# Kernel tuning notes

Measured on AMD Instinct MI355X. Metric: run time of the kernel, lower is better.

Reference implementation:

```python
import jax, jax.numpy as jnp
import numpy as np

DIM = 768
HEADS = 12
DH = DIM // HEADS  # 64


def setup_inputs() -> dict:
    key = jax.random.key(0)
    k1, k2, k3, k4, k5 = jax.random.split(key, 5)
    b, p = 16, 1024
    x = jax.random.normal(k1, (b, p, DIM), dtype=jnp.float32)
    # torch nn.Linear params: W [out, in], b [out]
    s_qkv = 1.0 / np.sqrt(DIM)
    Wqkv = jax.random.uniform(k2, (3 * DIM, DIM), jnp.float32, -s_qkv, s_qkv)
    bqkv = jax.random.uniform(k3, (3 * DIM,), jnp.float32, -s_qkv, s_qkv)
    Wo = jax.random.uniform(k4, (DIM, DIM), jnp.float32, -s_qkv, s_qkv)
    bo = jax.random.uniform(k5, (DIM,), jnp.float32, -s_qkv, s_qkv)
    return {"x": x, "Wqkv": Wqkv, "bqkv": bqkv, "Wo": Wo, "bo": bo}


def reference(x, Wqkv, bqkv, Wo, bo):
    b, p, _ = x.shape
    qkv = x @ Wqkv.T + bqkv                      # [b, p, 3*dim]
    q, k, v = jnp.split(qkv, 3, axis=-1)
    def to_heads(t):
        return t.reshape(b, p, HEADS, DH).transpose(0, 2, 1, 3)  # [b, h, p, d]
    q, k, v = to_heads(q), to_heads(k), to_heads(v)
    A = jnp.einsum('bhqd,bhkd->bhqk', q, k) / jnp.sqrt(jnp.float32(DH))
    # NOTE: softmax over the QUERY axis (dim=2), not the key axis
    P = jax.nn.softmax(A, axis=2)                # [b, h, q, k]
    MSA = jnp.einsum('bhqk,bhkd->bhqd', P, v)    # [b, h, p, d]
    MSA = MSA.transpose(0, 2, 1, 3).reshape(b, p, DIM)
    return MSA @ Wo.T + bo
```

## Files before the change

### kernel.cpp

```cpp
#include <hip/hip_runtime.h>
#include <hip/hip_bf16.h>
#include <math.h>

#define DIMC 768
#define HEADS 12
#define DHD 64
#define NB 16
#define NP 1024
#define NQKV (3*DIMC)

typedef __attribute__((ext_vector_type(8))) short bf16x8;
typedef __attribute__((ext_vector_type(4))) float f32x4;

__device__ __forceinline__ short f2bf(float f){
  unsigned u = __builtin_bit_cast(unsigned, f);
  u = (u + 0x7fffu + ((u >> 16) & 1u)) >> 16;
  return (short)u;
}
__device__ __forceinline__ float bf2f(short s){
  return __builtin_bit_cast(float, ((unsigned)(unsigned short)s) << 16);
}
__device__ __forceinline__ bf16x8 cvt8(float4 a, float4 b){
  bf16x8 v;
  v[0]=f2bf(a.x); v[1]=f2bf(a.y); v[2]=f2bf(a.z); v[3]=f2bf(a.w);
  v[4]=f2bf(b.x); v[5]=f2bf(b.y); v[6]=f2bf(b.z); v[7]=f2bf(b.w);
  return v;
}
__device__ __forceinline__ void glds16(const void* gsrc, void* ldst){
  __builtin_amdgcn_global_load_lds(
      (const __attribute__((address_space(1))) unsigned int*)gsrc,
      (__attribute__((address_space(3))) unsigned int*)ldst, 16, 0, 0);
}
__device__ __forceinline__ int xcd_swz(int p, int nwg){
  return (p & 7) * (nwg >> 3) + (p >> 3);
}

__global__ __launch_bounds__(256) void cvt_bf16(const float* __restrict__ in, short* __restrict__ out, int n8)
{
  int i = blockIdx.x*256 + threadIdx.x;
  if (i < n8) {
    float4 f0 = ((const float4*)in)[i*2];
    float4 f1 = ((const float4*)in)[i*2+1];
    ((bf16x8*)out)[i] = cvt8(f0, f1);
  }
}

template<int OUTBF16, int QSCALE>
__global__ __launch_bounds__(256) void gemm_bt(
    const short* __restrict__ A, const short* __restrict__ B,
    const float* __restrict__ bias, void* __restrict__ Cp,
    int N, int K, int NX)
{
  __shared__ __align__(16) short As[128*32];
  __shared__ __align__(16) short Bs[128*32];
  const int l = xcd_swz(blockIdx.x, gridDim.x);
  const int bn = (l % NX) * 128, bm = (l / NX) * 128;
  const int t = threadIdx.x;
  const int lane = t & 63, w = t >> 6;
  const int wr = w >> 1, wc = w & 1;
  const int lr = lane & 15, lg = lane >> 4;
  const int srow = lane >> 2;
  const int acol = (lane & 3) * 8;

  f32x4 acc[4][4] = {};

  for (int k0 = 0; k0 < K; k0 += 32) {
    glds16(A + (size_t)(bm + w*32 +  0 + srow)*K + k0 + acol, &As[(w*32 +  0)*32]);
    glds16(A + (size_t)(bm + w*32 + 16 + srow)*K + k0 + acol, &As[(w*32 + 16)*32]);
    glds16(B + (size_t)(bn + w*32 +  0 + srow)*K + k0 + acol, &Bs[(w*32 +  0)*32]);
    glds16(B + (size_t)(bn + w*32 + 16 + srow)*K + k0 + acol, &Bs[(w*32 + 16)*32]);
    __syncthreads();
    bf16x8 a[4], b[4];
    #pragma unroll
    for (int i=0;i<4;i++) a[i] = *(const bf16x8*)&As[(wr*64 + i*16 + lr)*32 + lg*8];
    #pragma unroll
    for (int i=0;i<4;i++) b[i] = *(const bf16x8*)&Bs[(wc*64 + i*16 + lr)*32 + lg*8];
    #pragma unroll
    for (int mf=0;mf<4;mf++)
      #pragma unroll
      for (int nf=0;nf<4;nf++)
        acc[mf][nf] = __builtin_amdgcn_mfma_f32_16x16x32_bf16(a[mf], b[nf], acc[mf][nf], 0,0,0);
    __syncthreads();
  }
  #pragma unroll
  for (int nf=0;nf<4;nf++){
    const int n = bn + wc*64 + nf*16 + lr;
    const float bb = bias[n];
    const float sc = (QSCALE && n < DIMC) ? 0.18033688011112042f : 1.0f;
    #pragma unroll
    for (int mf=0;mf<4;mf++)
      #pragma unroll
      for (int i=0;i<4;i++){
        const int m = bm + wr*64 + mf*16 + lg*4 + i;
        const float v = (acc[mf][nf][i] + bb) * sc;
        if (OUTBF16) ((short*)Cp)[(size_t)m*N + n] = f2bf(v);
        else         ((float*)Cp)[(size_t)m*N + n] = v;
      }
  }
}

__global__ __launch_bounds__(256) void vtrans(const short* __restrict__ qkv,
                                              const float* __restrict__ invs,
                                              short* __restrict__ vT)
{
  __shared__ __align__(16) short Ts[64][72];
  __shared__ float invl[64];
  const int pt = blockIdx.x, h = blockIdx.y, b = blockIdx.z;
  const int t = threadIdx.x;
  const size_t bh = (size_t)(b*HEADS + h);
  if (t < 64) invl[t] = invs[bh*NP + pt*64 + t];
  {
    const int r = t >> 2, q = t & 3;
    const short* src = qkv + (size_t)(b*NP + pt*64 + r)*NQKV + 2*DIMC + h*DHD + q*16;
    *(bf16x8*)&Ts[r][q*16]   = *(const bf16x8*)src;
    *(bf16x8*)&Ts[r][q*16+8] = *(const bf16x8*)(src+8);
  }
  __syncthreads();
  {
    const int d = t >> 2, q = t & 3;
    __align__(16) short tmp[16];
    #pragma unroll
    for (int j=0;j<16;j++) tmp[j] = f2bf(bf2f(Ts[q*16 + j][d]) * invl[q*16 + j]);
    short* dst = vT + (bh*DHD + d)*NP + pt*64 + q*16;
    *(bf16x8*)dst     = *(bf16x8*)&tmp[0];
    *(bf16x8*)(dst+8) = *(bf16x8*)&tmp[8];
  }
}

__global__ __launch_bounds__(256) void col_stats(const short* __restrict__ qkv, float* __restrict__ invs)
{
  __shared__ __align__(16) short Ks[128][72];
  __shared__ __align__(16) short Qs[64][72];
  __shared__ float red[4][128];
  const int l = xcd_swz(blockIdx.x, gridDim.x);
  const int kc = l & 7, h = (l >> 3) % HEADS, b = l / (8*HEADS);
  const int t = threadIdx.x;
  const int lane = t & 63, w = t >> 6;
  const int lr = lane & 15, lg = lane >> 4, lk = lg*8;
  const size_t rowbase = (size_t)(b*NP)*NQKV + h*DHD;
  {
    const int r = t >> 1, half = t & 1;
    const short* src = qkv + rowbase + (size_t)(kc*128 + r)*NQKV + DIMC + half*32;
    #pragma unroll
    for (int c=0;c<4;c++)
      *(bf16x8*)&Ks[r][half*32 + c*8] = *(const bf16x8*)(src + c*8);
  }
  float rsum[8] = {};
  for (int qt=0; qt<16; qt++){
    __syncthreads();
    {
      const int r = t >> 2, q = t & 3;
      const short* src = qkv + rowbase + (size_t)(qt*64 + r)*NQKV + q*16;
      *(bf16x8*)&Qs[r][q*16]   = *(const bf16x8*)src;
      *(bf16x8*)&Qs[r][q*16+8] = *(const bf16x8*)(src+8);
    }
    __syncthreads();
    bf16x8 qa0 = *(const bf16x8*)&Qs[w*16 + lr][lk];
    bf16x8 qa1 = *(const bf16x8*)&Qs[w*16 + lr][32 + lk];
    #pragma unroll
    for (int kf=0; kf<8; kf++){
      f32x4 acc = {};
      bf16x8 kb0 = *(const bf16x8*)&Ks[kf*16 + lr][lk];
      bf16x8 kb1 = *(const bf16x8*)&Ks[kf*16 + lr][32 + lk];
      acc = __builtin_amdgcn_mfma_f32_16x16x32_bf16(qa0, kb0, acc, 0,0,0);
      acc = __builtin_amdgcn_mfma_f32_16x16x32_bf16(qa1, kb1, acc, 0,0,0);
      #pragma unroll
      for (int i=0;i<4;i++) rsum[kf] += __builtin_amdgcn_exp2f(acc[i]);
    }
  }
  #pragma unroll
  for (int kf=0;kf<8;kf++){
    float v = rsum[kf];
    v += __shfl_xor(v, 16);
    v += __shfl_xor(v, 32);
    if (lane < 16) red[w][kf*16 + lr] = v;
  }
  __syncthreads();
  if (t < 128) {
    float s = red[0][t] + red[1][t] + red[2][t] + red[3][t];
    invs[(size_t)(b*HEADS + h)*NP + kc*128 + t] = 1.0f / s;
  }
}

__global__ __launch_bounds__(256) void attn_pv(const short* __restrict__ qkv, const short* __restrict__ vT,
                                               short* __restrict__ msa)
{
  __shared__ __align__(16) short Ks[2][64*64];
  __shared__ __align__(16) short Vs[2][64*64];
  __shared__ __align__(16) short Ps[4][16][72];
  const int l = xcd_swz(blockIdx.x, gridDim.x);
  const int qt2 = l & 7, h = (l >> 3) % HEADS, b = l / (8*HEADS);
  const int t = threadIdx.x;
  const int lane = t & 63, w = t >> 6;
  const int lr = lane & 15, lg = lane >> 4;
  const size_t qkvbase = (size_t)(b*NP)*NQKV + h*DHD;
  const size_t bh = (size_t)(b*HEADS + h);
  bf16x8 qa[2][2];
  {
    const short* Qbase = qkv + qkvbase + (size_t)(qt2*128 + w*32 + lr)*NQKV + lg*8;
    #pragma unroll
    for (int g=0; g<2; g++)
      #pragma unroll
      for (int hh=0; hh<2; hh++)
        qa[g][hh] = *(const bf16x8*)(Qbase + (size_t)g*16*NQKV + hh*32);
  }
  const int srw = lane >> 3;
  const int scol = 8 * ((lane & 7) ^ srw);
  const int sx = (lr & 7) << 3;
  const short* kp = qkv + qkvbase + DIMC + (size_t)(w*16 + srw)*NQKV + scol;
  const short* vp = vT + bh*DHD*NP + (size_t)(w*16 + srw)*NP + scol;

  #define STAGE(buf, kt) do { \
    _Pragma("unroll") \
    for (int j=0; j<2; j++){ \
      glds16(kp + (size_t)((kt)*64 + j*8)*NQKV, &Ks[buf][(w*16 + j*8)*64]); \
      glds16(vp + (size_t)(j*8)*NP + (kt)*64,   &Vs[buf][(w*16 + j*8)*64]); \
    } } while(0)

  f32x4 o[2][4] = {};
  STAGE(0, 0);
  int cur = 0;
  for (int kt=0; kt<16; kt++){
    if (kt < 15) {
      STAGE(cur^1, kt+1);
      asm volatile("s_waitcnt vmcnt(4)" ::: "memory");
    } else {
      asm volatile("s_waitcnt vmcnt(0)" ::: "memory");
    }
    __builtin_amdgcn_s_barrier();
    #pragma unroll
    for (int g=0; g<2; g++){
      bf16x8 kb0, kb1;
      f32x4 s[4];
      __builtin_amdgcn_s_setprio(1);
      #pragma unroll
      for (int kf=0; kf<4; kf++){
        kb0 = *(const bf16x8*)&Ks[cur][(kf*16 + lr)*64 + ((     lg*8) ^ sx)];
        kb1 = *(const bf16x8*)&Ks[cur][(kf*16 + lr)*64 + ((32 + lg*8) ^ sx)];
        f32x4 z = {};
        z = __builtin_amdgcn_mfma_f32_16x16x32_bf16(kb0, qa[g][0], z, 0,0,0);
        s[kf] = __builtin_amdgcn_mfma_f32_16x16x32_bf16(kb1, qa[g][1], z, 0,0,0);
      }
      __builtin_amdgcn_s_setprio(0);
      #pragma unroll
      for (int kf=0; kf<4; kf++){
        float e0 = __builtin_amdgcn_exp2f(s[kf][0]);
        float e1 = __builtin_amdgcn_exp2f(s[kf][1]);
        float e2 = __builtin_amdgcn_exp2f(s[kf][2]);
        float e3 = __builtin_amdgcn_exp2f(s[kf][3]);
        unsigned u0, u1;
        asm("v_cvt_pk_bf16_f32 %0, %1, %2" : "=v"(u0) : "v"(e0), "v"(e1));
        asm("v_cvt_pk_bf16_f32 %0, %1, %2" : "=v"(u1) : "v"(e2), "v"(e3));
        uint2 uu; uu.x = u0; uu.y = u1;
        *(uint2*)&Ps[w][lr][kf*16 + lg*4] = uu;
      }
      bf16x8 pa0 = *(const bf16x8*)&Ps[w][lr][lg*8];
      bf16x8 pa1 = *(const bf16x8*)&Ps[w][lr][32 + lg*8];
      __builtin_amdgcn_s_setprio(1);
      #pragma unroll
      for (int df=0; df<4; df++){
        bf16x8 vb0 = *(const bf16x8*)&Vs[cur][(df*16 + lr)*64 + ((     lg*8) ^ sx)];
        bf16x8 vb1 = *(const bf16x8*)&Vs[cur][(df*16 + lr)*64 + ((32 + lg*8) ^ sx)];
        o[g][df] = __builtin_amdgcn_mfma_f32_16x16x32_bf16(pa0, vb0, o[g][df], 0,0,0);
        o[g][df] = __builtin_amdgcn_mfma_f32_16x16x32_bf16(pa1, vb1, o[g][df], 0,0,0);
      }
      __builtin_amdgcn_s_setprio(0);
    }
    __builtin_amdgcn_s_barrier();
    cur ^= 1;
  }
  #undef STAGE
  #pragma unroll
  for (int g=0; g<2; g++)
    #pragma unroll
    for (int df=0; df<4; df++){
      const int d = h*DHD + df*16 + lr;
      #pragma unroll
      for (int i=0;i<4;i++){
        const int p = qt2*128 + w*32 + g*16 + lg*4 + i;
        msa[((size_t)(b*NP) + p)*DIMC + d] = f2bf(o[g][df][i]);
      }
    }
}

extern "C" void kernel_launch(void* const* d_in, const int* in_sizes, int n_in,
                              void* d_out, int out_size, void* d_ws, size_t ws_size,
                              hipStream_t stream)
{
  const float* x    = (const float*)d_in[0];
  const float* Wqkv = (const float*)d_in[1];
  const float* bqkv = (const float*)d_in[2];
  const float* Wo   = (const float*)d_in[3];
  const float* bo   = (const float*)d_in[4];
  char* ws = (char*)d_ws;
  short* qkv   = (short*)ws;
  short* vT    = (short*)(ws + 75497472);
  short* Wqkvb = vT;
  short* msa   = (short*)(ws + 100663296);
  short* xb    = msa;
  float* invs  = (float*)(ws + 125829120);
  short* Wob   = qkv;

  cvt_bf16<<<6144, 256, 0, stream>>>(x, xb, (16384*768)/8);
  cvt_bf16<<<864, 256, 0, stream>>>(Wqkv, Wqkvb, (2304*768)/8);
  gemm_bt<1,1><<<2304, 256, 0, stream>>>(xb, Wqkvb, bqkv, qkv, NQKV, DIMC, 18);
  col_stats<<<1536, 256, 0, stream>>>(qkv, invs);
  vtrans<<<dim3(16, HEADS, NB), 256, 0, stream>>>(qkv, invs, vT);
  attn_pv<<<1536, 256, 0, stream>>>(qkv, vT, msa);
  cvt_bf16<<<288, 256, 0, stream>>>(Wo, Wob, (768*768)/8);
  gemm_bt<0,0><<<768, 256, 0, stream>>>(msa, Wob, bo, d_out, DIMC, DIMC, 6);
}
```

Before: 347.5 us.

## Double-buffer GEMM LDS tiles with XOR swizzle and MFMA priority

Adds a second LDS buffer to the bf16 GEMM so the global-to-LDS loads for the next K tile are issued while the current tile is being multiplied. Waits use explicit vmcnt counters and raw barriers instead of __syncthreads. Applies an XOR swizzle to the LDS column layout to reduce bank conflicts on fragment reads, and raises wave priority around the MFMA block. This doubles LDS use per block, which may lower occupancy, and relies on the hand-written vmcnt counts being correct.

```diff
diff --git a/kernel.cpp b/kernel.cpp
--- a/kernel.cpp
+++ b/kernel.cpp
@@ -51,37 +51,56 @@
     const float* __restrict__ bias, void* __restrict__ Cp,
     int N, int K, int NX)
 {
-  __shared__ __align__(16) short As[128*32];
-  __shared__ __align__(16) short Bs[128*32];
+  __shared__ __align__(16) short As[2][128*32];
+  __shared__ __align__(16) short Bs[2][128*32];
   const int l = xcd_swz(blockIdx.x, gridDim.x);
   const int bn = (l % NX) * 128, bm = (l / NX) * 128;
   const int t = threadIdx.x;
   const int lane = t & 63, w = t >> 6;
   const int wr = w >> 1, wc = w & 1;
   const int lr = lane & 15, lg = lane >> 4;
-  const int srow = lane >> 2;
-  const int acol = (lane & 3) * 8;
+  const int srw = lane >> 2;
+  const int acol = 8 * ((lane & 3) ^ ((lane >> 3) & 3));
+  const int rsx = (lr >> 1) & 3;
+
+  const short* ap = A + (size_t)(bm + w*32 + srw)*K + acol;
+  const short* bp = B + (size_t)(bn + w*32 + srw)*K + acol;
+
+  #define GSTAGE(buf, k0) do { \
+    glds16(ap + (k0),        &As[buf][(w*32 +  0)*32]); \
+    glds16(ap + 16*K + (k0), &As[buf][(w*32 + 16)*32]); \
+    glds16(bp + (k0),        &Bs[buf][(w*32 +  0)*32]); \
+    glds16(bp + 16*K + (k0), &Bs[buf][(w*32 + 16)*32]); \
+  } while(0)
 
   f32x4 acc[4][4] = {};
-
-  for (int k0 = 0; k0 < K; k0 += 32) {
-    glds16(A + (size_t)(bm + w*32 +  0 + srow)*K + k0 + acol, &As[(w*32 +  0)*32]);
-    glds16(A + (size_t)(bm + w*32 + 16 + srow)*K + k0 + acol, &As[(w*32 + 16)*32]);
-    glds16(B + (size_t)(bn + w*32 +  0 + srow)*K + k0 + acol, &Bs[(w*32 +  0)*32]);
-    glds16(B + (size_t)(bn + w*32 + 16 + srow)*K + k0 + acol, &Bs[(w*32 + 16)*32]);
-    __syncthreads();
+  const int nk = K >> 5;
+  GSTAGE(0, 0);
+  int cur = 0;
+  for (int kt = 0; kt < nk; ++kt) {
+    if (kt + 1 < nk) {
+      GSTAGE(cur^1, (kt+1)*32);
+      asm volatile("s_waitcnt vmcnt(4)" ::: "memory");
+    } else {
+      asm volatile("s_waitcnt vmcnt(0)" ::: "memory");
+    }
+    __builtin_amdgcn_s_barrier();
     bf16x8 a[4], b[4];
     #pragma unroll
-    for (int i=0;i<4;i++) a[i] = *(const bf16x8*)&As[(wr*64 + i*16 + lr)*32 + lg*8];
-    #pragma unroll
-    for (int i=0;i<4;i++) b[i] = *(const bf16x8*)&Bs[(wc*64 + i*16 + lr)*32 + lg*8];
+    for (int i=0;i<4;i++) a[i] = *(const bf16x8*)&As[cur][(wr*64 + i*16 + lr)*32 + (lg ^ rsx)*8];
+    #pragma unroll
+    for (int i=0;i<4;i++) b[i] = *(const bf16x8*)&Bs[cur][(wc*64 + i*16 + lr)*32 + (lg ^ rsx)*8];
+    __builtin_amdgcn_s_setprio(1);
     #pragma unroll
     for (int mf=0;mf<4;mf++)
       #pragma unroll
       for (int nf=0;nf<4;nf++)
         acc[mf][nf] = __builtin_amdgcn_mfma_f32_16x16x32_bf16(a[mf], b[nf], acc[mf][nf], 0,0,0);
-    __syncthreads();
-  }
+    __builtin_amdgcn_s_setprio(0);
+    __builtin_amdgcn_s_barrier();
+    cur ^= 1;
+  }
+  #undef GSTAGE
   #pragma unroll
   for (int nf=0;nf<4;nf++){
     const int n = bn + wc*64 + nf*16 + lr;
```

Result: no change. 345.7 us (-0.5%).
